# Kernel tuning notes

Hardware: AMD Instinct MI355X
Metric: run time of the kernel (lower is better)

The kernel has to match this reference:

```python
import jax, jax.numpy as jnp
import numpy as np

TEMP = 1.0

def setup_inputs() -> dict:
    key = jax.random.key(0)
    k1, k2, k3, k4 = jax.random.split(key, 4)
    B, Q, K, H = 8, 1024, 4096, 512
    output = jax.random.normal(k1, (B, Q, H), dtype=jnp.float32)
    context = jax.random.normal(k2, (B, K, H), dtype=jnp.float32)
    mask = jax.random.randint(k3, (B, Q, K), 0, 2).astype(jnp.bool_)
    # linear_out: Linear(2H -> H), torch layout W: [H, 2H]
    W_out = jax.random.normal(k4, (H, 2 * H), dtype=jnp.float32) * (1.0 / np.sqrt(2 * H))
    b_out = jnp.zeros((H,), dtype=jnp.float32)
    return {"output": output, "context": context, "mask": mask, "W_out": W_out, "b_out": b_out}

def reference(output, context, mask, W_out, b_out):
    # attn scores: [B, Q, K]
    attn = jnp.einsum('bqh,bkh->bqk', output, context)
    attn = jnp.where(mask, -jnp.inf, attn)
    attn = jax.nn.softmax(attn / TEMP, axis=-1)
    # mix: [B, Q, H]
    mix = jnp.einsum('bqk,bkh->bqh', attn, context)
    combined = jnp.concatenate([mix, output], axis=-1)  # [B, Q, 2H]
    out = jnp.tanh(jnp.einsum('bqc,hc->bqh', combined, W_out) + b_out)
    return (out, attn)
```

## Files before the change

### kernel.cpp

```cpp
#include <hip/hip_runtime.h>
#include <cstdint>
#include <cstddef>

#define B_N 8
#define Q_N 1024
#define K_N 4096
#define H_N 512
#define C_N 1024
#define R_N (B_N * Q_N)

typedef short bf16x8 __attribute__((ext_vector_type(8)));
typedef float f32x4 __attribute__((ext_vector_type(4)));

typedef const void __attribute__((address_space(1))) gas_void;
typedef void __attribute__((address_space(3))) las_void;

__device__ __forceinline__ unsigned short f2bf(float f) {
    union { float f; unsigned u; } v; v.f = f;
    unsigned u = v.u;
    u += 0x7FFFu + ((u >> 16) & 1u);
    return (unsigned short)(u >> 16);
}
__device__ __forceinline__ float bf2f(unsigned short h) {
    union { unsigned u; float f; } v; v.u = ((unsigned)h) << 16;
    return v.f;
}

__device__ __forceinline__ f32x4 mfma16(bf16x8 a, bf16x8 b, f32x4 c) {
    return __builtin_amdgcn_mfma_f32_16x16x32_bf16(a, b, c, 0, 0, 0);
}

__global__ void k_split(const float* __restrict__ x, unsigned short* __restrict__ hi,
                        unsigned short* __restrict__ lo, int n4) {
    int i = blockIdx.x * 256 + threadIdx.x;
    if (i >= n4) return;
    float4 v = reinterpret_cast<const float4*>(x)[i];
    ushort4 h, l;
    h.x = f2bf(v.x); l.x = f2bf(v.x - bf2f(h.x));
    h.y = f2bf(v.y); l.y = f2bf(v.y - bf2f(h.y));
    h.z = f2bf(v.z); l.z = f2bf(v.z - bf2f(h.z));
    h.w = f2bf(v.w); l.w = f2bf(v.w - bf2f(h.w));
    reinterpret_cast<ushort4*>(hi)[i] = h;
    reinterpret_cast<ushort4*>(lo)[i] = l;
}

__global__ void k_cvt(const float* __restrict__ x, unsigned short* __restrict__ hi, int n4) {
    int i = blockIdx.x * 256 + threadIdx.x;
    if (i >= n4) return;
    float4 v = reinterpret_cast<const float4*>(x)[i];
    ushort4 h;
    h.x = f2bf(v.x); h.y = f2bf(v.y); h.z = f2bf(v.z); h.w = f2bf(v.w);
    reinterpret_cast<ushort4*>(hi)[i] = h;
}

__global__ __launch_bounds__(256)
void k_prep_ctx(const float* __restrict__ ctx, unsigned short* __restrict__ ctxHi,
                unsigned short* __restrict__ ctxLo, unsigned short* __restrict__ ctxT) {
    __shared__ unsigned short tile[64][66];
    const int b = blockIdx.z;
    const int k0 = blockIdx.x * 64;
    const int h0 = blockIdx.y * 64;
    const int tx = threadIdx.x & 15;
    const int ty = threadIdx.x >> 4;
#pragma unroll
    for (int r = 0; r < 64; r += 16) {
        const int k = ty + r;
        const size_t go = ((size_t)b * K_N + k0 + k) * H_N + h0 + tx * 4;
        float4 v = *reinterpret_cast<const float4*>(ctx + go);
        ushort4 h, l;
        h.x = f2bf(v.x); l.x = f2bf(v.x - bf2f(h.x));
        h.y = f2bf(v.y); l.y = f2bf(v.y - bf2f(h.y));
        h.z = f2bf(v.z); l.z = f2bf(v.z - bf2f(h.z));
        h.w = f2bf(v.w); l.w = f2bf(v.w - bf2f(h.w));
        *reinterpret_cast<ushort4*>(ctxHi + go) = h;
        *reinterpret_cast<ushort4*>(ctxLo + go) = l;
        tile[tx * 4 + 0][k] = h.x;
        tile[tx * 4 + 1][k] = h.y;
        tile[tx * 4 + 2][k] = h.z;
        tile[tx * 4 + 3][k] = h.w;
    }
    __syncthreads();
#pragma unroll
    for (int r = 0; r < 64; r += 16) {
        const int h = ty + r;
        ushort4 t4 = *reinterpret_cast<const ushort4*>(&tile[h][tx * 4]);
        *reinterpret_cast<ushort4*>(ctxT + ((size_t)b * H_N + h0 + h) * K_N + k0 + tx * 4) = t4;
    }
}

__device__ __forceinline__ void stage_tile(const unsigned short* __restrict__ g, int ld,
                                           unsigned short* __restrict__ lds) {
    const int t = threadIdx.x;
    const int wbase = t & ~63;
#pragma unroll
    for (int i = 0; i < 2; i++) {
        int idx = i * 256 + t;
        const unsigned short* ga = g + (size_t)(idx >> 2) * ld + (idx & 3) * 8;
        unsigned short* la = lds + (size_t)(i * 256 + wbase) * 8;
        __builtin_amdgcn_global_load_lds((gas_void*)ga, (las_void*)la, 16, 0, 0);
    }
}

__global__ __launch_bounds__(256, 2)
void k_scores(const unsigned short* __restrict__ outHi, const unsigned short* __restrict__ outLo,
              const unsigned short* __restrict__ ctxHi, const unsigned short* __restrict__ ctxLo,
              const int* __restrict__ mask, float* __restrict__ S) {
    __shared__ unsigned short Ah[128 * 32], Al[128 * 32], Bh[128 * 32], Bl[128 * 32];
    const int b = blockIdx.z;
    const int q0 = blockIdx.y * 128;
    const int k0 = blockIdx.x * 128;
    const unsigned short* Ahg = outHi + ((size_t)b * Q_N + q0) * H_N;
    const unsigned short* Alg = outLo + ((size_t)b * Q_N + q0) * H_N;
    const unsigned short* Bhg = ctxHi + ((size_t)b * K_N + k0) * H_N;
    const unsigned short* Blg = ctxLo + ((size_t)b * K_N + k0) * H_N;
    const int lane = threadIdx.x & 63;
    const int w = threadIdx.x >> 6;
    const int wr = (w >> 1) * 64;
    const int wc = (w & 1) * 64;
    const int fm = lane & 15;
    const int fg = (lane >> 4) * 8;

    f32x4 acc[4][4];
#pragma unroll
    for (int i = 0; i < 4; i++)
#pragma unroll
        for (int j = 0; j < 4; j++) acc[i][j] = (f32x4){0.f, 0.f, 0.f, 0.f};

    for (int kc = 0; kc < H_N; kc += 32) {
        stage_tile(Ahg + kc, H_N, Ah);
        stage_tile(Alg + kc, H_N, Al);
        stage_tile(Bhg + kc, H_N, Bh);
        stage_tile(Blg + kc, H_N, Bl);
        __syncthreads();
        bf16x8 ah[4], al[4], bh[4], bl[4];
#pragma unroll
        for (int i = 0; i < 4; i++) {
            ah[i] = *(const bf16x8*)&Ah[(wr + i * 16 + fm) * 32 + fg];
            al[i] = *(const bf16x8*)&Al[(wr + i * 16 + fm) * 32 + fg];
            bh[i] = *(const bf16x8*)&Bh[(wc + i * 16 + fm) * 32 + fg];
            bl[i] = *(const bf16x8*)&Bl[(wc + i * 16 + fm) * 32 + fg];
        }
#pragma unroll
        for (int i = 0; i < 4; i++)
#pragma unroll
            for (int j = 0; j < 4; j++) {
                acc[i][j] = mfma16(ah[i], bh[j], acc[i][j]);
                acc[i][j] = mfma16(ah[i], bl[j], acc[i][j]);
                acc[i][j] = mfma16(al[i], bh[j], acc[i][j]);
            }
        __syncthreads();
    }
    float* Sb = S + (size_t)b * Q_N * K_N;
    const int orow = (lane >> 4) * 4;
    const int ocol = lane & 15;
#pragma unroll
    for (int i = 0; i < 4; i++)
#pragma unroll
        for (int r = 0; r < 4; r++) {
            int q = q0 + wr + i * 16 + orow + r;
            const size_t rowoff = (size_t)q * K_N + (k0 + wc + ocol);
            float* dst = Sb + rowoff;
            const int* mrow = mask + (size_t)b * Q_N * K_N + rowoff;
#pragma unroll
            for (int j = 0; j < 4; j++) {
                float v = acc[i][j][r];
                dst[j * 16] = mrow[j * 16] ? -1e30f : v;
            }
        }
}

__global__ __launch_bounds__(256)
void k_softmax(float* __restrict__ S, unsigned short* __restrict__ pbf) {
    const size_t r = blockIdx.x;
    float* row = S + r * K_N;
    unsigned short* prow = pbf + r * K_N;
    const int t = threadIdx.x;

    float4 v[4];
    float lmax = -1e30f;
#pragma unroll
    for (int i = 0; i < 4; i++) {
        int idx = i * 256 + t;
        float4 s = reinterpret_cast<const float4*>(row)[idx];
        v[i] = s;
        lmax = fmaxf(fmaxf(fmaxf(lmax, s.x), fmaxf(s.y, s.z)), s.w);
    }
#pragma unroll
    for (int off = 32; off >= 1; off >>= 1)
        lmax = fmaxf(lmax, __shfl_xor(lmax, off, 64));
    __shared__ float redm[4];
    __shared__ float reds[4];
    const int wv = t >> 6;
    if ((t & 63) == 0) redm[wv] = lmax;
    __syncthreads();
    const float m = fmaxf(fmaxf(redm[0], redm[1]), fmaxf(redm[2], redm[3]));

    float4 e[4];
    float lsum = 0.f;
#pragma unroll
    for (int i = 0; i < 4; i++) {
        e[i].x = __expf(v[i].x - m);
        e[i].y = __expf(v[i].y - m);
        e[i].z = __expf(v[i].z - m);
        e[i].w = __expf(v[i].w - m);
        lsum += (e[i].x + e[i].y) + (e[i].z + e[i].w);
    }
#pragma unroll
    for (int off = 32; off >= 1; off >>= 1)
        lsum += __shfl_xor(lsum, off, 64);
    if ((t & 63) == 0) reds[wv] = lsum;
    __syncthreads();
    const float inv = 1.0f / (reds[0] + reds[1] + reds[2] + reds[3]);

#pragma unroll
    for (int i = 0; i < 4; i++) {
        int idx = i * 256 + t;
        float4 p;
        p.x = e[i].x * inv; p.y = e[i].y * inv; p.z = e[i].z * inv; p.w = e[i].w * inv;
        reinterpret_cast<float4*>(row)[idx] = p;
        ushort4 pb;
        pb.x = f2bf(p.x); pb.y = f2bf(p.y); pb.z = f2bf(p.z); pb.w = f2bf(p.w);
        reinterpret_cast<ushort4*>(prow)[idx] = pb;
    }
}

__global__ __launch_bounds__(256, 2)
void k_mix(const unsigned short* __restrict__ P, const unsigned short* __restrict__ ctxT,
           unsigned short* __restrict__ mixBf) {
    __shared__ unsigned short A0[128 * 32], A1[128 * 32], B0[128 * 32], B1[128 * 32];
    const int b = blockIdx.z;
    const int q0 = blockIdx.y * 128;
    const int h0 = blockIdx.x * 128;
    const unsigned short* Ag = P + ((size_t)b * Q_N + q0) * K_N;
    const unsigned short* Bg = ctxT + ((size_t)b * H_N + h0) * K_N;
    const int lane = threadIdx.x & 63;
    const int w = threadIdx.x >> 6;
    const int wr = (w >> 1) * 64;
    const int wc = (w & 1) * 64;
    const int fm = lane & 15;
    const int fg = (lane >> 4) * 8;

    f32x4 acc[4][4];
#pragma unroll
    for (int i = 0; i < 4; i++)
#pragma unroll
        for (int j = 0; j < 4; j++) acc[i][j] = (f32x4){0.f, 0.f, 0.f, 0.f};

    for (int kc = 0; kc < K_N; kc += 64) {
        stage_tile(Ag + kc, K_N, A0);
        stage_tile(Ag + kc + 32, K_N, A1);
        stage_tile(Bg + kc, K_N, B0);
        stage_tile(Bg + kc + 32, K_N, B1);
        __syncthreads();
        bf16x8 a[4], bb[4];
#pragma unroll
        for (int i = 0; i < 4; i++) {
            a[i] = *(const bf16x8*)&A0[(wr + i * 16 + fm) * 32 + fg];
            bb[i] = *(const bf16x8*)&B0[(wc + i * 16 + fm) * 32 + fg];
        }
#pragma unroll
        for (int i = 0; i < 4; i++)
#pragma unroll
            for (int j = 0; j < 4; j++) acc[i][j] = mfma16(a[i], bb[j], acc[i][j]);
#pragma unroll
        for (int i = 0; i < 4; i++) {
            a[i] = *(const bf16x8*)&A1[(wr + i * 16 + fm) * 32 + fg];
            bb[i] = *(const bf16x8*)&B1[(wc + i * 16 + fm) * 32 + fg];
        }
#pragma unroll
        for (int i = 0; i < 4; i++)
#pragma unroll
            for (int j = 0; j < 4; j++) acc[i][j] = mfma16(a[i], bb[j], acc[i][j]);
        __syncthreads();
    }
    const int orow = (lane >> 4) * 4;
    const int ocol = lane & 15;
#pragma unroll
    for (int i = 0; i < 4; i++)
#pragma unroll
        for (int r = 0; r < 4; r++) {
            int q = q0 + wr + i * 16 + orow + r;
            unsigned short* dst = mixBf + ((size_t)b * Q_N + q) * H_N + (h0 + wc + ocol);
#pragma unroll
            for (int j = 0; j < 4; j++) dst[j * 16] = f2bf(acc[i][j][r]);
        }
}

__global__ __launch_bounds__(256, 2)
void k_outlin(const unsigned short* __restrict__ mixBf, const unsigned short* __restrict__ outHi,
              const unsigned short* __restrict__ Whi, const float* __restrict__ bias,
              float* __restrict__ out) {
    __shared__ unsigned short At[128 * 32], Bt[128 * 32];
    const int r0 = blockIdx.y * 128;
    const int h0 = blockIdx.x * 128;
    const int lane = threadIdx.x & 63;
    const int w = threadIdx.x >> 6;
    const int wr = (w >> 1) * 64;
    const int wc = (w & 1) * 64;
    const int fm = lane & 15;
    const int fg = (lane >> 4) * 8;

    f32x4 acc[4][4];
#pragma unroll
    for (int i = 0; i < 4; i++)
#pragma unroll
        for (int j = 0; j < 4; j++) acc[i][j] = (f32x4){0.f, 0.f, 0.f, 0.f};

    for (int kc = 0; kc < C_N; kc += 32) {
        const unsigned short* Ag = (kc < H_N)
            ? mixBf + (size_t)r0 * H_N + kc
            : outHi + (size_t)r0 * H_N + (kc - H_N);
        stage_tile(Ag, H_N, At);
        stage_tile(Whi + (size_t)h0 * C_N + kc, C_N, Bt);
        __syncthreads();
        bf16x8 a[4], bb[4];
#pragma unroll
        for (int i = 0; i < 4; i++) {
            a[i] = *(const bf16x8*)&At[(wr + i * 16 + fm) * 32 + fg];
            bb[i] = *(const bf16x8*)&Bt[(wc + i * 16 + fm) * 32 + fg];
        }
#pragma unroll
        for (int i = 0; i < 4; i++)
#pragma unroll
            for (int j = 0; j < 4; j++) acc[i][j] = mfma16(a[i], bb[j], acc[i][j]);
        __syncthreads();
    }
    const int orow = (lane >> 4) * 4;
    const int ocol = lane & 15;
#pragma unroll
    for (int i = 0; i < 4; i++)
#pragma unroll
        for (int r = 0; r < 4; r++) {
            int rr = r0 + wr + i * 16 + orow + r;
#pragma unroll
            for (int j = 0; j < 4; j++) {
                int h = h0 + wc + j * 16 + ocol;
                float v = acc[i][j][r] + bias[h];
                out[(size_t)rr * H_N + h] = tanhf(v);
            }
        }
}

extern "C" void kernel_launch(void* const* d_in, const int* in_sizes, int n_in,
                              void* d_out, int out_size, void* d_ws, size_t ws_size,
                              hipStream_t stream) {
    const float* d_output  = (const float*)d_in[0];
    const float* d_context = (const float*)d_in[1];
    const int*   d_mask    = (const int*)d_in[2];
    const float* d_W       = (const float*)d_in[3];
    const float* d_bias    = (const float*)d_in[4];

    float* out_res = (float*)d_out;
    float* attn    = out_res + (size_t)R_N * H_N;

    char* ws = (char*)d_ws;
    unsigned short* ctxHi = (unsigned short*)ws; ws += (size_t)B_N * K_N * H_N * 2;
    unsigned short* ctxLo = (unsigned short*)ws; ws += (size_t)B_N * K_N * H_N * 2;
    unsigned short* ctxT  = (unsigned short*)ws; ws += (size_t)B_N * K_N * H_N * 2;
    unsigned short* outHi = (unsigned short*)ws; ws += (size_t)R_N * H_N * 2;
    unsigned short* outLo = (unsigned short*)ws; ws += (size_t)R_N * H_N * 2;
    unsigned short* Whi   = (unsigned short*)ws; ws += (size_t)H_N * C_N * 2;
    unsigned short* pBf   = (unsigned short*)ws; ws += (size_t)R_N * K_N * 2;
    unsigned short* mixBf = (unsigned short*)ws; ws += (size_t)R_N * H_N * 2;

    k_split<<<dim3((R_N * H_N / 4) / 256), 256, 0, stream>>>(d_output, outHi, outLo, R_N * H_N / 4);
    k_cvt<<<dim3((H_N * C_N / 4) / 256), 256, 0, stream>>>(d_W, Whi, H_N * C_N / 4);
    k_prep_ctx<<<dim3(K_N / 64, H_N / 64, B_N), 256, 0, stream>>>(d_context, ctxHi, ctxLo, ctxT);

    k_scores<<<dim3(K_N / 128, Q_N / 128, B_N), 256, 0, stream>>>(outHi, outLo, ctxHi, ctxLo,
                                                                  d_mask, attn);

    k_softmax<<<dim3(R_N), 256, 0, stream>>>(attn, pBf);

    k_mix<<<dim3(H_N / 128, Q_N / 128, B_N), 256, 0, stream>>>(pBf, ctxT, mixBf);

    k_outlin<<<dim3(H_N / 128, R_N / 128), 256, 0, stream>>>(mixBf, outHi, Whi, d_bias, out_res);
}
```

Baseline: 589.5 us.

## Move mask into softmax and halve N tile of mix and outlin GEMMs

The mask is now applied inside the softmax kernel, loaded as vectorized int4 per row, instead of through scalar strided loads in the scores epilogue. The mix and output-linear GEMMs switch from 128x128 to 128x64 block tiles, with each wave owning 32 rows. This doubles their grid sizes: k_mix goes from 256 to 512 blocks and k_outlin from 256 to 512, giving better CU occupancy across the device. In exchange there is less operand reuse per block and more redundant A-tile loads.

```diff
diff --git a/kernel.cpp b/kernel.cpp
--- a/kernel.cpp
+++ b/kernel.cpp
@@ -100,11 +100,18 @@
         __builtin_amdgcn_global_load_lds((gas_void*)ga, (las_void*)la, 16, 0, 0);
     }
 }
+__device__ __forceinline__ void stage_tile64(const unsigned short* __restrict__ g, int ld,
+                                             unsigned short* __restrict__ lds) {
+    const int t = threadIdx.x;
+    const unsigned short* ga = g + (size_t)(t >> 2) * ld + (t & 3) * 8;
+    unsigned short* la = lds + (size_t)(t & ~63) * 8;
+    __builtin_amdgcn_global_load_lds((gas_void*)ga, (las_void*)la, 16, 0, 0);
+}
 
 __global__ __launch_bounds__(256, 2)
 void k_scores(const unsigned short* __restrict__ outHi, const unsigned short* __restrict__ outLo,
               const unsigned short* __restrict__ ctxHi, const unsigned short* __restrict__ ctxLo,
-              const int* __restrict__ mask, float* __restrict__ S) {
+              float* __restrict__ S) {
     __shared__ unsigned short Ah[128 * 32], Al[128 * 32], Bh[128 * 32], Bl[128 * 32];
     const int b = blockIdx.z;
     const int q0 = blockIdx.y * 128;
@@ -158,21 +165,17 @@
 #pragma unroll
         for (int r = 0; r < 4; r++) {
             int q = q0 + wr + i * 16 + orow + r;
-            const size_t rowoff = (size_t)q * K_N + (k0 + wc + ocol);
-            float* dst = Sb + rowoff;
-            const int* mrow = mask + (size_t)b * Q_N * K_N + rowoff;
-#pragma unroll
-            for (int j = 0; j < 4; j++) {
-                float v = acc[i][j][r];
-                dst[j * 16] = mrow[j * 16] ? -1e30f : v;
-            }
+            float* dst = Sb + (size_t)q * K_N + (k0 + wc + ocol);
+#pragma unroll
+            for (int j = 0; j < 4; j++) dst[j * 16] = acc[i][j][r];
         }
 }
 
 __global__ __launch_bounds__(256)
-void k_softmax(float* __restrict__ S, unsigned short* __restrict__ pbf) {
+void k_softmax(float* __restrict__ S, const int* __restrict__ mask, unsigned short* __restrict__ pbf) {
     const size_t r = blockIdx.x;
     float* row = S + r * K_N;
+    const int* mrow = mask + r * K_N;
     unsigned short* prow = pbf + r * K_N;
     const int t = threadIdx.x;
 
@@ -182,6 +185,11 @@
     for (int i = 0; i < 4; i++) {
         int idx = i * 256 + t;
         float4 s = reinterpret_cast<const float4*>(row)[idx];
+        int4 mk = reinterpret_cast<const int4*>(mrow)[idx];
+        s.x = mk.x ? -1e30f : s.x;
+        s.y = mk.y ? -1e30f : s.y;
+        s.z = mk.z ? -1e30f : s.z;
+        s.w = mk.w ? -1e30f : s.w;
         v[i] = s;
         lmax = fmaxf(fmaxf(fmaxf(lmax, s.x), fmaxf(s.y, s.z)), s.w);
     }
@@ -227,48 +235,45 @@
 __global__ __launch_bounds__(256, 2)
 void k_mix(const unsigned short* __restrict__ P, const unsigned short* __restrict__ ctxT,
            unsigned short* __restrict__ mixBf) {
-    __shared__ unsigned short A0[128 * 32], A1[128 * 32], B0[128 * 32], B1[128 * 32];
+    __shared__ unsigned short A0[128 * 32], A1[128 * 32], B0[64 * 32], B1[64 * 32];
     const int b = blockIdx.z;
     const int q0 = blockIdx.y * 128;
-    const int h0 = blockIdx.x * 128;
+    const int h0 = blockIdx.x * 64;
     const unsigned short* Ag = P + ((size_t)b * Q_N + q0) * K_N;
     const unsigned short* Bg = ctxT + ((size_t)b * H_N + h0) * K_N;
     const int lane = threadIdx.x & 63;
     const int w = threadIdx.x >> 6;
-    const int wr = (w >> 1) * 64;
-    const int wc = (w & 1) * 64;
+    const int wr = w * 32;
     const int fm = lane & 15;
     const int fg = (lane >> 4) * 8;
 
-    f32x4 acc[4][4];
-#pragma unroll
-    for (int i = 0; i < 4; i++)
+    f32x4 acc[2][4];
+#pragma unroll
+    for (int i = 0; i < 2; i++)
 #pragma unroll
         for (int j = 0; j < 4; j++) acc[i][j] = (f32x4){0.f, 0.f, 0.f, 0.f};
 
     for (int kc = 0; kc < K_N; kc += 64) {
         stage_tile(Ag + kc, K_N, A0);
         stage_tile(Ag + kc + 32, K_N, A1);
-        stage_tile(Bg + kc, K_N, B0);
-        stage_tile(Bg + kc + 32, K_N, B1);
-        __syncthreads();
-        bf16x8 a[4], bb[4];
-#pragma unroll
-        for (int i = 0; i < 4; i++) {
-            a[i] = *(const bf16x8*)&A0[(wr + i * 16 + fm) * 32 + fg];
-            bb[i] = *(const bf16x8*)&B0[(wc + i * 16 + fm) * 32 + fg];
-        }
-#pragma unroll
-        for (int i = 0; i < 4; i++)
+        stage_tile64(Bg + kc, K_N, B0);
+        stage_tile64(Bg + kc + 32, K_N, B1);
+        __syncthreads();
+        bf16x8 a[2], bb[4];
+#pragma unroll
+        for (int i = 0; i < 2; i++) a[i] = *(const bf16x8*)&A0[(wr + i * 16 + fm) * 32 + fg];
+#pragma unroll
+        for (int j = 0; j < 4; j++) bb[j] = *(const bf16x8*)&B0[(j * 16 + fm) * 32 + fg];
+#pragma unroll
+        for (int i = 0; i < 2; i++)
 #pragma unroll
             for (int j = 0; j < 4; j++) acc[i][j] = mfma16(a[i], bb[j], acc[i][j]);
 #pragma unroll
-        for (int i = 0; i < 4; i++) {
-            a[i] = *(const bf16x8*)&A1[(wr + i * 16 + fm) * 32 + fg];
-            bb[i] = *(const bf16x8*)&B1[(wc + i * 16 + fm) * 32 + fg];
-        }
-#pragma unroll
-        for (int i = 0; i < 4; i++)
+        for (int i = 0; i < 2; i++) a[i] = *(const bf16x8*)&A1[(wr + i * 16 + fm) * 32 + fg];
+#pragma unroll
+        for (int j = 0; j < 4; j++) bb[j] = *(const bf16x8*)&B1[(j * 16 + fm) * 32 + fg];
+#pragma unroll
+        for (int i = 0; i < 2; i++)
 #pragma unroll
             for (int j = 0; j < 4; j++) acc[i][j] = mfma16(a[i], bb[j], acc[i][j]);
         __syncthreads();
@@ -276,11 +281,11 @@
     const int orow = (lane >> 4) * 4;
     const int ocol = lane & 15;
 #pragma unroll
-    for (int i = 0; i < 4; i++)
+    for (int i = 0; i < 2; i++)
 #pragma unroll
         for (int r = 0; r < 4; r++) {
             int q = q0 + wr + i * 16 + orow + r;
-            unsigned short* dst = mixBf + ((size_t)b * Q_N + q) * H_N + (h0 + wc + ocol);
+            unsigned short* dst = mixBf + ((size_t)b * Q_N + q) * H_N + (h0 + ocol);
 #pragma unroll
             for (int j = 0; j < 4; j++) dst[j * 16] = f2bf(acc[i][j][r]);
         }
@@ -290,19 +295,18 @@
 void k_outlin(const unsigned short* __restrict__ mixBf, const unsigned short* __restrict__ outHi,
               const unsigned short* __restrict__ Whi, const float* __restrict__ bias,
               float* __restrict__ out) {
-    __shared__ unsigned short At[128 * 32], Bt[128 * 32];
+    __shared__ unsigned short At[128 * 32], Bt[64 * 32];
     const int r0 = blockIdx.y * 128;
-    const int h0 = blockIdx.x * 128;
+    const int h0 = blockIdx.x * 64;
     const int lane = threadIdx.x & 63;
     const int w = threadIdx.x >> 6;
-    const int wr = (w >> 1) * 64;
-    const int wc = (w & 1) * 64;
+    const int wr = w * 32;
     const int fm = lane & 15;
     const int fg = (lane >> 4) * 8;
 
-    f32x4 acc[4][4];
-#pragma unroll
-    for (int i = 0; i < 4; i++)
+    f32x4 acc[2][4];
+#pragma unroll
+    for (int i = 0; i < 2; i++)
 #pragma unroll
         for (int j = 0; j < 4; j++) acc[i][j] = (f32x4){0.f, 0.f, 0.f, 0.f};
 
@@ -311,16 +315,15 @@
             ? mixBf + (size_t)r0 * H_N + kc
             : outHi + (size_t)r0 * H_N + (kc - H_N);
         stage_tile(Ag, H_N, At);
-        stage_tile(Whi + (size_t)h0 * C_N + kc, C_N, Bt);
-        __syncthreads();
-        bf16x8 a[4], bb[4];
-#pragma unroll
-        for (int i = 0; i < 4; i++) {
-            a[i] = *(const bf16x8*)&At[(wr + i * 16 + fm) * 32 + fg];
-            bb[i] = *(const bf16x8*)&Bt[(wc + i * 16 + fm) * 32 + fg];
-        }
-#pragma unroll
-        for (int i = 0; i < 4; i++)
+        stage_tile64(Whi + (size_t)h0 * C_N + kc, C_N, Bt);
+        __syncthreads();
+        bf16x8 a[2], bb[4];
+#pragma unroll
+        for (int i = 0; i < 2; i++) a[i] = *(const bf16x8*)&At[(wr + i * 16 + fm) * 32 + fg];
+#pragma unroll
+        for (int j = 0; j < 4; j++) bb[j] = *(const bf16x8*)&Bt[(j * 16 + fm) * 32 + fg];
+#pragma unroll
+        for (int i = 0; i < 2; i++)
 #pragma unroll
             for (int j = 0; j < 4; j++) acc[i][j] = mfma16(a[i], bb[j], acc[i][j]);
         __syncthreads();
@@ -328,13 +331,13 @@
     const int orow = (lane >> 4) * 4;
     const int ocol = lane & 15;
 #pragma unroll
-    for (int i = 0; i < 4; i++)
+    for (int i = 0; i < 2; i++)
 #pragma unroll
         for (int r = 0; r < 4; r++) {
             int rr = r0 + wr + i * 16 + orow + r;
 #pragma unroll
             for (int j = 0; j < 4; j++) {
-                int h = h0 + wc + j * 16 + ocol;
+                int h = h0 + j * 16 + ocol;
                 float v = acc[i][j][r] + bias[h];
                 out[(size_t)rr * H_N + h] = tanhf(v);
             }
@@ -367,12 +370,11 @@
     k_cvt<<<dim3((H_N * C_N / 4) / 256), 256, 0, stream>>>(d_W, Whi, H_N * C_N / 4);
     k_prep_ctx<<<dim3(K_N / 64, H_N / 64, B_N), 256, 0, stream>>>(d_context, ctxHi, ctxLo, ctxT);
 
-    k_scores<<<dim3(K_N / 128, Q_N / 128, B_N), 256, 0, stream>>>(outHi, outLo, ctxHi, ctxLo,
-                                                                  d_mask, attn);
-
-    k_softmax<<<dim3(R_N), 256, 0, stream>>>(attn, pBf);
-
-    k_mix<<<dim3(H_N / 128, Q_N / 128, B_N), 256, 0, stream>>>(pBf, ctxT, mixBf);
-
-    k_outlin<<<dim3(H_N / 128, R_N / 128), 256, 0, stream>>>(mixBf, outHi, Whi, d_bias, out_res);
-}
+    k_scores<<<dim3(K_N / 128, Q_N / 128, B_N), 256, 0, stream>>>(outHi, outLo, ctxHi, ctxLo, attn);
+
+    k_softmax<<<dim3(R_N), 256, 0, stream>>>(attn, d_mask, pBf);
+
+    k_mix<<<dim3(H_N / 64, Q_N / 128, B_N), 256, 0, stream>>>(pBf, ctxT, mixBf);
+
+    k_outlin<<<dim3(H_N / 64, R_N / 128), 256, 0, stream>>>(mixBf, outHi, Whi, d_bias, out_res);
+}
```

New measurement: 557.2 us. 5.5% less time.
